# Performance work log

Measured on AMD Instinct MI355X. Metric: run time of the kernel, lower is better.

## Reference

```python
import jax, jax.numpy as jnp
import numpy as np

R_GAS = 8314.46261815324   # Cantera gas constant, J/(kmol K)
ONE_ATM = 101325.0
B, S, NR = 2048, 100, 800
POLY = 5


def setup_inputs() -> dict:
    key = jax.random.key(0)
    ks = jax.random.split(key, 11)
    T = jax.random.uniform(ks[0], (B, 1), minval=300.0, maxval=2500.0)
    P = ONE_ATM * jax.random.uniform(ks[1], (B, 1), minval=0.5, maxval=2.0)
    Y = jax.random.uniform(ks[2], (B, S), minval=0.01, maxval=1.0)
    TPY = jnp.concatenate([T, P, Y], axis=1)
    molecular_weights = jax.random.uniform(ks[3], (S, 1), minval=2.0, maxval=100.0)
    # NASA-7 coefficients with realistic per-column magnitudes
    scales = jnp.array([1.0, 1e-3, 1e-6, 1e-9, 1e-12, 1e3, 1.0])
    base = jnp.array([3.5, 0.0, 0.0, 0.0, 0.0, 0.0, 5.0])
    nasa_low = jax.random.normal(ks[4], (S, 7)) * scales + base
    nasa_high = jax.random.normal(ks[5], (S, 7)) * scales + base
    efficiencies_coeffs = jax.random.uniform(ks[6], (S, NR), minval=0.0, maxval=2.0)
    is_three_body = (jax.random.uniform(ks[7], (NR,)) < 0.3).astype(jnp.float32)
    # positive poly coefficients so viscosity/conductivity/diffusion stay > 0
    species_viscosities_poly = jax.random.uniform(ks[8], (POLY, S), minval=1e-6, maxval=1e-5)
    thermal_conductivity_poly = jax.random.uniform(ks[9], (POLY, S), minval=1e-4, maxval=1e-3)
    binary_diff_coeffs_poly = jax.random.uniform(ks[10], (POLY, S * S), minval=1e-7, maxval=1e-6)
    return {
        'TPY': TPY,
        'molecular_weights': molecular_weights,
        'nasa_low': nasa_low,
        'nasa_high': nasa_high,
        'efficiencies_coeffs': efficiencies_coeffs,
        'is_three_body': is_three_body,
        'species_viscosities_poly': species_viscosities_poly,
        'thermal_conductivity_poly': thermal_conductivity_poly,
        'binary_diff_coeffs_poly': binary_diff_coeffs_poly,
    }


def _forward(TPY, mw, nasa_low, nasa_high, eff, i3b, visc_poly, cond_poly, bdiff_poly):
    n_sp = mw.shape[0]
    # ---- set_states: state variables ----
    T = jnp.clip(TPY[:, 0:1], 200.0, None)            # [B,1]
    logT = jnp.log(T)
    P = TPY[:, 1:2]
    Y = jnp.clip(TPY[:, 2:], 0.0, None)
    Y = Y / Y.sum(axis=1, keepdims=True)
    mean_W = 1.0 / (Y @ (1.0 / mw))                   # [B,1]
    rho = P / R_GAS / T * mean_W                      # mass density
    X = Y * mean_W / mw.T                             # mole fractions
    C = Y * rho / mw.T                                # molar concentrations
    mask = (T <= 1000.0).astype(T.dtype)              # [B,1] NASA branch select
    # ---- cp (NASA poly) ----
    cp_T = jnp.concatenate([T**0, T, T**2, T**3, T**4], axis=1)
    cp = (cp_T @ nasa_low[:, :5].T) * mask + (cp_T @ nasa_high[:, :5].T) * (1.0 - mask)
    cp_mole = (R_GAS * cp * X).sum(axis=1)
    # ---- enthalpy ----
    H_T = jnp.concatenate([T**0, T / 2, T**2 / 3, T**3 / 4, T**4 / 5, 1.0 / T], axis=1)
    H = ((H_T @ nasa_low[:, :6].T) * mask + (H_T @ nasa_high[:, :6].T) * (1.0 - mask)) * R_GAS * T
    h = H / mw.T
    enthalpy_mass = (h * Y).sum(axis=1)
    # ---- entropy ----
    idx = jnp.array([0, 1, 2, 3, 4, 6])
    S_T = jnp.concatenate([logT, T, T**2 / 2, T**3 / 3, T**4 / 4, T**0], axis=1)
    S0 = ((S_T @ nasa_low[:, idx].T) * mask + (S_T @ nasa_high[:, idx].T) * (1.0 - mask)) * R_GAS
    S_sp = S0 - R_GAS * jnp.log(X) - R_GAS * jnp.log(P / ONE_ATM)
    s = S_sp / mw.T
    entropy_mass = (s * Y).sum(axis=1)
    # ---- third-body effective concentrations ----
    C_M = C @ eff                                     # [B,NR]
    C_M2 = C_M * i3b + (1.0 - i3b)
    # ---- update_transport: viscosity (Wilke mixing) ----
    poly_order = visc_poly.shape[0]
    trans_T = jnp.concatenate([logT**i for i in range(poly_order - 1, -1, -1)], axis=1)
    sp_visc = trans_T @ visc_poly                     # [B,S]
    Wk_over_Wj = mw @ (1.0 / mw.T)                    # [S,S]
    Wj_over_Wk = 1.0 / Wk_over_Wj
    eta_ratio = sp_visc[:, :, None] / sp_visc[:, None, :]  # [B,S,S]
    PHI = (1.0 / 2.8284271247461903) / jnp.sqrt(1.0 + Wk_over_Wj) \
          * (1.0 + jnp.sqrt(eta_ratio) * Wj_over_Wk**0.25) ** 2
    denom = jnp.einsum('bij,bj->bi', PHI, X)
    viscosities = (X * sp_visc / denom).sum(axis=1, keepdims=True)
    # ---- thermal conductivity ----
    sp_cond = trans_T @ cond_poly
    thermal_conductivity = 0.5 * ((X * sp_cond).sum(axis=1, keepdims=True)
                                  + 1.0 / (X / sp_cond).sum(axis=1, keepdims=True))
    # ---- mixture-averaged diffusion coefficients ----
    bdc = (trans_T @ bdiff_poly).reshape(-1, n_sp, n_sp)    # [B,S,S]
    X_eps = jnp.clip(X, 1e-12, None)
    XjWj = X_eps @ mw - X_eps * mw.T                        # [B,S]
    XjDjk = jnp.einsum('bj,bjk->bk', X_eps, 1.0 / bdc) \
            - X_eps / jnp.diagonal(bdc, axis1=-2, axis2=-1)
    mix_diff = XjWj / XjDjk / mean_W / P * ONE_ATM
    return jnp.concatenate([cp_mole[:, None], enthalpy_mass[:, None], entropy_mass[:, None],
                            C_M2, viscosities, thermal_conductivity, mix_diff], axis=1)


def reference(TPY, molecular_weights, nasa_low, nasa_high, efficiencies_coeffs,
              is_three_body, species_viscosities_poly, thermal_conductivity_poly,
              binary_diff_coeffs_poly):
    return _forward(TPY, molecular_weights, nasa_low, nasa_high, efficiencies_coeffs,
                    is_three_body, species_viscosities_poly, thermal_conductivity_poly,
                    binary_diff_coeffs_poly)
```

## Files before the change

### kernel.cpp

```cpp
#include <hip/hip_runtime.h>
#include <math.h>

namespace {

constexpr int S = 100;
constexpr int NR = 800;
constexpr int RPB = 4;
constexpr int NTH = 512;
constexpr int IN_COLS = 2 + S;
constexpr int OUT_COLS = 3 + NR + 2 + S;
constexpr float RGASF = 8314.46261815324f;
constexpr float ATMF = 101325.0f;
constexpr size_t PHI_WS_BYTES = 3 * 10000 * sizeof(float);

__device__ __forceinline__ float wave_sum(float v) {
#pragma unroll
  for (int off = 32; off; off >>= 1) v += __shfl_xor(v, off);
  return v;
}

__device__ __forceinline__ float elem(const float4& v, int i) {
  return ((const float*)&v)[i];
}

__global__ __launch_bounds__(256)
void phi_precompute(const float* __restrict__ mw, float* __restrict__ pm) {
  int idx = blockIdx.x * 256 + threadIdx.x;
  if (idx >= 10000) return;
  int i = idx / 100, k = idx % 100;
  float mwi = mw[i], mwk = mw[k];
  float A = 0.35355339059327373f *
            __builtin_amdgcn_rsqf(1.0f + mwi * __builtin_amdgcn_rcpf(mwk));
  float B4 = __builtin_amdgcn_exp2f(0.25f * (__log2f(mwk) - __log2f(mwi)));
  pm[idx] = A;
  pm[10000 + idx] = A * B4;
  pm[20000 + idx] = A * B4 * B4;
}

template <bool PRE>
__global__ __launch_bounds__(NTH, 8)
void chem_props_kernel(const float* __restrict__ TPY,
                       const float* __restrict__ mw,
                       const float* __restrict__ nasa_low,
                       const float* __restrict__ nasa_high,
                       const float* __restrict__ eff,
                       const float* __restrict__ i3b,
                       const float* __restrict__ visc_poly,
                       const float* __restrict__ cond_poly,
                       const float* __restrict__ bdiff_poly,
                       const float* __restrict__ pm,
                       float* __restrict__ out)
{
  __shared__ __align__(16) float4 XL[S];
  __shared__ __align__(16) float4 U1[S];
  __shared__ __align__(16) float4 U2[S];
  __shared__ __align__(16) float4 VL[S];
  __shared__ float mwl[S];
  __shared__ float2 ilm[S];
  __shared__ float pa[8][2];
  __shared__ float pb[8][5];
  __shared__ float rs_L[RPB], rs_cfac[RPB], rs_mW[RPB], rs_scale[RPB], rs_T[RPB];
  __shared__ float psum[2][RPB];
  __shared__ __align__(16) float xjd[50][RPB];

  const int tid = threadIdx.x;
  const int wid = tid >> 6;
  const int lane = tid & 63;
  const int h = blockIdx.x & 1;
  const int row0 = (blockIdx.x >> 1) * RPB;

  if (tid < S) {
    float m = mw[tid];
    mwl[tid] = m;
    ilm[tid] = make_float2(1.0f / m, __log2f(m));
  }
  __syncthreads();

  const int row = wid & 3;
  const int half = wid >> 2;
  const float* rowp = TPY + (size_t)(row0 + row) * IN_COLS;
  float T = fmaxf(rowp[0], 200.0f);
  float P = rowp[1];
  float L = __logf(T);
  const int s = half * 64 + lane;
  const bool valid = (s < S);
  float y = valid ? fmaxf(rowp[2 + s], 0.0f) : 0.0f;
  float im = valid ? ilm[s].x : 0.0f;
  {
    float py = wave_sum(y);
    float pw = wave_sum(y * im);
    if (lane == 0) { pa[wid][0] = py; pa[wid][1] = pw; }
  }
  __syncthreads();
  {
    float T2 = T * T, T3 = T2 * T, T4 = T2 * T2;
    float invT = 1.0f / T;
    float ysum = pa[row][0] + pa[row + 4][0];
    float wsum = pa[row][1] + pa[row + 4][1];
    float invy = 1.0f / ysum;
    float mW = ysum / wsum;
    float cfac = P / (RGASF * T);
    float lnP = __logf(P * (1.0f / ATMF));
    const float* nasa = (T <= 1000.0f) ? nasa_low : nasa_high;

    float cpx = 0.0f, hy = 0.0f, sy = 0.0f, condA = 0.0f, condB = 0.0f;
    if (valid) {
      float yn = y * invy;
      float x = fmaxf(yn * mW * im, 1e-12f);
      const float* a = nasa + s * 7;
      float a0 = a[0], a1 = a[1], a2 = a[2], a3 = a[3],
            a4 = a[4], a5 = a[5], a6 = a[6];
      float cp = a0 + a1 * T + a2 * T2 + a3 * T3 + a4 * T4;
      float Ht = a0 + 0.5f * a1 * T + (1.0f / 3.0f) * a2 * T2
               + 0.25f * a3 * T3 + 0.2f * a4 * T4 + a5 * invT;
      float S0r = a0 * L + a1 * T + 0.5f * a2 * T2
                + (1.0f / 3.0f) * a3 * T3 + 0.25f * a4 * T4 + a6;
      cpx = cp * x;
      hy = Ht * im * yn;
      sy = (S0r - __logf(x) - lnP) * im * yn;

      float v = visc_poly[0 * S + s];
      v = fmaf(v, L, visc_poly[1 * S + s]);
      v = fmaf(v, L, visc_poly[2 * S + s]);
      v = fmaf(v, L, visc_poly[3 * S + s]);
      v = fmaf(v, L, visc_poly[4 * S + s]);
      float c = cond_poly[0 * S + s];
      c = fmaf(c, L, cond_poly[1 * S + s]);
      c = fmaf(c, L, cond_poly[2 * S + s]);
      c = fmaf(c, L, cond_poly[3 * S + s]);
      c = fmaf(c, L, cond_poly[4 * S + s]);
      condA = x * c;
      condB = x / c;
      ((float*)&XL[s])[row] = x;
      ((float*)&VL[s])[row] = v;
      ((float*)&U1[s])[row] = x * __builtin_amdgcn_rsqf(v);
      ((float*)&U2[s])[row] = x * __builtin_amdgcn_rcpf(v);
    }
    float scp = wave_sum(cpx);
    float sh = wave_sum(hy);
    float ss = wave_sum(sy);
    float sca = wave_sum(condA);
    float scb = wave_sum(condB);
    if (lane == 0) {
      pb[wid][0] = scp; pb[wid][1] = sh; pb[wid][2] = ss;
      pb[wid][3] = sca; pb[wid][4] = scb;
      if (half == 0) {
        rs_L[row] = L;
        rs_T[row] = T;
        rs_cfac[row] = cfac;
        rs_mW[row] = mW;
        rs_scale[row] = ATMF / (mW * P);
      }
    }
  }
  __syncthreads();

  if (h == 0 && tid < RPB) {
    const int r = tid;
    float scp = pb[r][0] + pb[r + 4][0];
    float sh  = pb[r][1] + pb[r + 4][1];
    float ss  = pb[r][2] + pb[r + 4][2];
    float sca = pb[r][3] + pb[r + 4][3];
    float scb = pb[r][4] + pb[r + 4][4];
    float* orow = out + (size_t)(row0 + r) * OUT_COLS;
    orow[0] = RGASF * scp;
    orow[1] = RGASF * rs_T[r] * sh;
    orow[2] = RGASF * ss;
    orow[3 + NR + 1] = 0.5f * (sca + 1.0f / scb);
  }

  if (tid < 200) {
    const int q0 = h * 400 + tid * 2;
    float acc[2][RPB];
#pragma unroll
    for (int qi = 0; qi < 2; ++qi)
#pragma unroll
      for (int b = 0; b < RPB; ++b) acc[qi][b] = 0.0f;
#pragma unroll 4
    for (int s2 = 0; s2 < S; ++s2) {
      float2 e = *(const float2*)&eff[(size_t)s2 * NR + q0];
      float4 xq = XL[s2];
#pragma unroll
      for (int b = 0; b < RPB; ++b) {
        acc[0][b] = fmaf(elem(xq, b), e.x, acc[0][b]);
        acc[1][b] = fmaf(elem(xq, b), e.y, acc[1][b]);
      }
    }
    float2 t3 = *(const float2*)&i3b[q0];
#pragma unroll
    for (int qi = 0; qi < 2; ++qi) {
      float tq = qi ? t3.y : t3.x;
      float base = 1.0f - tq;
#pragma unroll
      for (int b = 0; b < RPB; ++b)
        out[(size_t)(row0 + b) * OUT_COLS + 3 + q0 + qi] =
            fmaf(acc[qi][b] * rs_cfac[b], tq, base);
    }
  } else if (tid >= 256 && tid < 384 && h == 0) {
    const int i = tid - 256;
    float contrib[RPB] = {0.0f, 0.0f, 0.0f, 0.0f};
    if (i < S) {
      float d0[RPB], d1[RPB], d2[RPB];
#pragma unroll
      for (int b = 0; b < RPB; ++b) { d0[b] = 0; d1[b] = 0; d2[b] = 0; }
      if (PRE) {
        const float* pm0 = pm + i * 100;
        const float* pm1 = pm + 10000 + i * 100;
        const float* pm2 = pm + 20000 + i * 100;
#pragma unroll 2
        for (int k4 = 0; k4 < S; k4 += 4) {
          float4 a0q = *(const float4*)&pm0[k4];
          float4 a1q = *(const float4*)&pm1[k4];
          float4 a2q = *(const float4*)&pm2[k4];
#pragma unroll
          for (int kk = 0; kk < 4; ++kk) {
            float4 xq = XL[k4 + kk];
            float4 u1q = U1[k4 + kk];
            float4 u2q = U2[k4 + kk];
            float m0 = elem(a0q, kk), m1 = elem(a1q, kk), m2 = elem(a2q, kk);
#pragma unroll
            for (int b = 0; b < RPB; ++b) {
              d0[b] = fmaf(m0, elem(xq, b), d0[b]);
              d1[b] = fmaf(m1, elem(u1q, b), d1[b]);
              d2[b] = fmaf(m2, elem(u2q, b), d2[b]);
            }
          }
        }
      } else {
        const float mwi = mwl[i];
        const float lmi = ilm[i].y;
#pragma unroll 4
        for (int k = 0; k < S; ++k) {
          float2 il = ilm[k];
          float A = 0.35355339059327373f *
                    __builtin_amdgcn_rsqf(1.0f + mwi * il.x);
          float B4 = __builtin_amdgcn_exp2f(0.25f * (il.y - lmi));
          float m1 = A * B4, m2 = m1 * B4;
          float4 xq = XL[k];
          float4 u1q = U1[k];
          float4 u2q = U2[k];
#pragma unroll
          for (int b = 0; b < RPB; ++b) {
            d0[b] = fmaf(A, elem(xq, b), d0[b]);
            d1[b] = fmaf(m1, elem(u1q, b), d1[b]);
            d2[b] = fmaf(m2, elem(u2q, b), d2[b]);
          }
        }
      }
      float4 vq = VL[i];
      float4 xiq = XL[i];
#pragma unroll
      for (int b = 0; b < RPB; ++b) {
        float vi = elem(vq, b);
        float den = d0[b] + 2.0f * sqrtf(vi) * d1[b] + vi * d2[b];
        contrib[b] = elem(xiq, b) * vi * __builtin_amdgcn_rcpf(den);
      }
    }
#pragma unroll
    for (int b = 0; b < RPB; ++b) contrib[b] = wave_sum(contrib[b]);
    if (lane == 0) {
#pragma unroll
      for (int b = 0; b < RPB; ++b) psum[wid - 4][b] = contrib[b];
    }
  } else if (tid >= 384 && tid < 484) {
    const int td = tid - 384;
    const int kk = td % 50;
    const int jh = td / 50;
    const int k = h * 50 + kk;
    const int j0 = jh * 50;
    float Lb[RPB], acc4[RPB];
#pragma unroll
    for (int b = 0; b < RPB; ++b) { Lb[b] = rs_L[b]; acc4[b] = 0.0f; }
    const float* bp = bdiff_poly + k;
#pragma unroll 2
    for (int j = j0; j < j0 + 50; ++j) {
      float c0 = bp[j * 100];
      float c1 = bp[10000 + j * 100];
      float c2 = bp[20000 + j * 100];
      float c3 = bp[30000 + j * 100];
      float c4 = bp[40000 + j * 100];
      float4 xq = XL[j];
      const bool diag = (j == k);
#pragma unroll
      for (int b = 0; b < RPB; ++b) {
        float p = fmaf(c0, Lb[b], c1);
        p = fmaf(p, Lb[b], c2);
        p = fmaf(p, Lb[b], c3);
        p = fmaf(p, Lb[b], c4);
        float r = diag ? 0.0f : __builtin_amdgcn_rcpf(p);
        acc4[b] = fmaf(elem(xq, b), r, acc4[b]);
      }
    }
    if (jh == 0) {
#pragma unroll
      for (int b = 0; b < RPB; ++b) xjd[kk][b] = acc4[b];
    } else {
#pragma unroll
      for (int b = 0; b < RPB; ++b) Lb[b] = acc4[b];
    }
    __syncthreads();
    if (jh == 1) {
      float4 xkq = XL[k];
      float mwk = mwl[k];
#pragma unroll
      for (int b = 0; b < RPB; ++b) {
        float tot = xjd[kk][b] + Lb[b];
        float num = rs_mW[b] - elem(xkq, b) * mwk;
        out[(size_t)(row0 + b) * OUT_COLS + 3 + NR + 2 + k] =
            num * __builtin_amdgcn_rcpf(tot) * rs_scale[b];
      }
    }
    return;
  }
  __syncthreads();

  if (h == 0 && tid < RPB) {
    out[(size_t)(row0 + tid) * OUT_COLS + 3 + NR] =
        psum[0][tid] + psum[1][tid];
  }
}

}

extern "C" void kernel_launch(void* const* d_in, const int* in_sizes, int n_in,
                              void* d_out, int out_size, void* d_ws, size_t ws_size,
                              hipStream_t stream) {
  const float* TPY        = (const float*)d_in[0];
  const float* mwp        = (const float*)d_in[1];
  const float* nasa_low   = (const float*)d_in[2];
  const float* nasa_high  = (const float*)d_in[3];
  const float* eff        = (const float*)d_in[4];
  const float* i3b        = (const float*)d_in[5];
  const float* visc_poly  = (const float*)d_in[6];
  const float* cond_poly  = (const float*)d_in[7];
  const float* bdiff_poly = (const float*)d_in[8];
  float* out = (float*)d_out;
  float* pm  = (float*)d_ws;

  const int B = 2048;
  dim3 grid((B / RPB) * 2);
  if (ws_size >= PHI_WS_BYTES) {
    phi_precompute<<<40, 256, 0, stream>>>(mwp, pm);
    chem_props_kernel<true><<<grid, NTH, 0, stream>>>(
        TPY, mwp, nasa_low, nasa_high, eff, i3b,
        visc_poly, cond_poly, bdiff_poly, pm, out);
  } else {
    chem_props_kernel<false><<<grid, NTH, 0, stream>>>(
        TPY, mwp, nasa_low, nasa_high, eff, i3b,
        visc_poly, cond_poly, bdiff_poly, nullptr, out);
  }
}
```

Baseline: 121.2 us.

## Merge half-blocks into one 1024-thread block with atomic diffusion reduction

Replaces the two-blocks-per-row-group split with a single 1024-thread block per four rows. The prologue work (species sums, NASA thermo, viscosity prep) is no longer duplicated across two blocks. The efficiency matvec, viscosity sum and diffusion sum now run concurrently in disjoint thread ranges. The diffusion sum is split four ways over j and reduced through shared-memory atomics into a full 100-species buffer before a final output pass. Larger blocks may reduce occupancy and leave wave slots idle, and the atomics add contention.

```diff
diff --git a/kernel.cpp b/kernel.cpp
--- a/kernel.cpp
+++ b/kernel.cpp
@@ -6,7 +6,7 @@
 constexpr int S = 100;
 constexpr int NR = 800;
 constexpr int RPB = 4;
-constexpr int NTH = 512;
+constexpr int NTH = 1024;
 constexpr int IN_COLS = 2 + S;
 constexpr int OUT_COLS = 3 + NR + 2 + S;
 constexpr float RGASF = 8314.46261815324f;
@@ -61,14 +61,14 @@
   __shared__ float pb[8][5];
   __shared__ float rs_L[RPB], rs_cfac[RPB], rs_mW[RPB], rs_scale[RPB], rs_T[RPB];
   __shared__ float psum[2][RPB];
-  __shared__ __align__(16) float xjd[50][RPB];
+  __shared__ __align__(16) float xjd[S][RPB];
 
   const int tid = threadIdx.x;
   const int wid = tid >> 6;
   const int lane = tid & 63;
-  const int h = blockIdx.x & 1;
-  const int row0 = (blockIdx.x >> 1) * RPB;
-
+  const int row0 = blockIdx.x * RPB;
+
+  if (tid < S * RPB) (&xjd[0][0])[tid] = 0.0f;
   if (tid < S) {
     float m = mw[tid];
     mwl[tid] = m;
@@ -76,23 +76,26 @@
   }
   __syncthreads();
 
-  const int row = wid & 3;
-  const int half = wid >> 2;
-  const float* rowp = TPY + (size_t)(row0 + row) * IN_COLS;
-  float T = fmaxf(rowp[0], 200.0f);
-  float P = rowp[1];
-  float L = __logf(T);
-  const int s = half * 64 + lane;
-  const bool valid = (s < S);
-  float y = valid ? fmaxf(rowp[2 + s], 0.0f) : 0.0f;
-  float im = valid ? ilm[s].x : 0.0f;
-  {
+  float T = 0.f, P = 0.f, L = 0.f, y = 0.f, im = 0.f;
+  int row = 0, half = 0, s = 0;
+  bool valid = false;
+  if (wid < 8) {
+    row = wid & 3;
+    half = wid >> 2;
+    const float* rowp = TPY + (size_t)(row0 + row) * IN_COLS;
+    T = fmaxf(rowp[0], 200.0f);
+    P = rowp[1];
+    L = __logf(T);
+    s = half * 64 + lane;
+    valid = (s < S);
+    y = valid ? fmaxf(rowp[2 + s], 0.0f) : 0.0f;
+    im = valid ? ilm[s].x : 0.0f;
     float py = wave_sum(y);
     float pw = wave_sum(y * im);
     if (lane == 0) { pa[wid][0] = py; pa[wid][1] = pw; }
   }
   __syncthreads();
-  {
+  if (wid < 8) {
     float T2 = T * T, T3 = T2 * T, T4 = T2 * T2;
     float invT = 1.0f / T;
     float ysum = pa[row][0] + pa[row + 4][0];
@@ -155,7 +158,7 @@
   }
   __syncthreads();
 
-  if (h == 0 && tid < RPB) {
+  if (tid < RPB) {
     const int r = tid;
     float scp = pb[r][0] + pb[r + 4][0];
     float sh  = pb[r][1] + pb[r + 4][1];
@@ -169,35 +172,31 @@
     orow[3 + NR + 1] = 0.5f * (sca + 1.0f / scb);
   }
 
-  if (tid < 200) {
-    const int q0 = h * 400 + tid * 2;
-    float acc[2][RPB];
-#pragma unroll
-    for (int qi = 0; qi < 2; ++qi)
-#pragma unroll
-      for (int b = 0; b < RPB; ++b) acc[qi][b] = 0.0f;
+  if (tid < 400) {
+    const int q0 = tid * 2;
+    float acc0[RPB], acc1[RPB];
+#pragma unroll
+    for (int b = 0; b < RPB; ++b) { acc0[b] = 0.0f; acc1[b] = 0.0f; }
 #pragma unroll 4
     for (int s2 = 0; s2 < S; ++s2) {
       float2 e = *(const float2*)&eff[(size_t)s2 * NR + q0];
       float4 xq = XL[s2];
 #pragma unroll
       for (int b = 0; b < RPB; ++b) {
-        acc[0][b] = fmaf(elem(xq, b), e.x, acc[0][b]);
-        acc[1][b] = fmaf(elem(xq, b), e.y, acc[1][b]);
+        acc0[b] = fmaf(elem(xq, b), e.x, acc0[b]);
+        acc1[b] = fmaf(elem(xq, b), e.y, acc1[b]);
       }
     }
     float2 t3 = *(const float2*)&i3b[q0];
-#pragma unroll
-    for (int qi = 0; qi < 2; ++qi) {
-      float tq = qi ? t3.y : t3.x;
-      float base = 1.0f - tq;
-#pragma unroll
-      for (int b = 0; b < RPB; ++b)
-        out[(size_t)(row0 + b) * OUT_COLS + 3 + q0 + qi] =
-            fmaf(acc[qi][b] * rs_cfac[b], tq, base);
-    }
-  } else if (tid >= 256 && tid < 384 && h == 0) {
-    const int i = tid - 256;
+    float base0 = 1.0f - t3.x, base1 = 1.0f - t3.y;
+#pragma unroll
+    for (int b = 0; b < RPB; ++b) {
+      float* op = out + (size_t)(row0 + b) * OUT_COLS + 3 + q0;
+      op[0] = fmaf(acc0[b] * rs_cfac[b], t3.x, base0);
+      op[1] = fmaf(acc1[b] * rs_cfac[b], t3.y, base1);
+    }
+  } else if (tid >= 448 && tid < 576) {
+    const int i = tid - 448;
     float contrib[RPB] = {0.0f, 0.0f, 0.0f, 0.0f};
     if (i < S) {
       float d0[RPB], d1[RPB], d2[RPB];
@@ -260,20 +259,19 @@
     for (int b = 0; b < RPB; ++b) contrib[b] = wave_sum(contrib[b]);
     if (lane == 0) {
 #pragma unroll
-      for (int b = 0; b < RPB; ++b) psum[wid - 4][b] = contrib[b];
-    }
-  } else if (tid >= 384 && tid < 484) {
-    const int td = tid - 384;
-    const int kk = td % 50;
-    const int jh = td / 50;
-    const int k = h * 50 + kk;
-    const int j0 = jh * 50;
+      for (int b = 0; b < RPB; ++b) psum[wid - 7][b] = contrib[b];
+    }
+  } else if (tid >= 576 && tid < 976) {
+    const int t = tid - 576;
+    const int k = t % 100;
+    const int jg = t / 100;
+    const int j0 = jg * 25;
     float Lb[RPB], acc4[RPB];
 #pragma unroll
     for (int b = 0; b < RPB; ++b) { Lb[b] = rs_L[b]; acc4[b] = 0.0f; }
     const float* bp = bdiff_poly + k;
-#pragma unroll 2
-    for (int j = j0; j < j0 + 50; ++j) {
+#pragma unroll 5
+    for (int j = j0; j < j0 + 25; ++j) {
       float c0 = bp[j * 100];
       float c1 = bp[10000 + j * 100];
       float c2 = bp[20000 + j * 100];
@@ -291,32 +289,25 @@
         acc4[b] = fmaf(elem(xq, b), r, acc4[b]);
       }
     }
-    if (jh == 0) {
-#pragma unroll
-      for (int b = 0; b < RPB; ++b) xjd[kk][b] = acc4[b];
-    } else {
-#pragma unroll
-      for (int b = 0; b < RPB; ++b) Lb[b] = acc4[b];
-    }
-    __syncthreads();
-    if (jh == 1) {
-      float4 xkq = XL[k];
-      float mwk = mwl[k];
-#pragma unroll
-      for (int b = 0; b < RPB; ++b) {
-        float tot = xjd[kk][b] + Lb[b];
-        float num = rs_mW[b] - elem(xkq, b) * mwk;
-        out[(size_t)(row0 + b) * OUT_COLS + 3 + NR + 2 + k] =
-            num * __builtin_amdgcn_rcpf(tot) * rs_scale[b];
-      }
-    }
-    return;
+#pragma unroll
+    for (int b = 0; b < RPB; ++b) atomicAdd(&xjd[k][b], acc4[b]);
   }
   __syncthreads();
 
-  if (h == 0 && tid < RPB) {
+  if (tid < RPB) {
     out[(size_t)(row0 + tid) * OUT_COLS + 3 + NR] =
         psum[0][tid] + psum[1][tid];
+  }
+  if (tid < S) {
+    const int k = tid;
+    float4 xkq = XL[k];
+    float mwk = mwl[k];
+#pragma unroll
+    for (int b = 0; b < RPB; ++b) {
+      float num = rs_mW[b] - elem(xkq, b) * mwk;
+      out[(size_t)(row0 + b) * OUT_COLS + 3 + NR + 2 + k] =
+          num * __builtin_amdgcn_rcpf(xjd[k][b]) * rs_scale[b];
+    }
   }
 }
 
@@ -338,7 +329,7 @@
   float* pm  = (float*)d_ws;
 
   const int B = 2048;
-  dim3 grid((B / RPB) * 2);
+  dim3 grid(B / RPB);
   if (ws_size >= PHI_WS_BYTES) {
     phi_precompute<<<40, 256, 0, stream>>>(mwp, pm);
     chem_props_kernel<true><<<grid, NTH, 0, stream>>>(
```

New measurement: 105.2 us. 13.2% less time.
